# Kernel tuning notes

Hardware: AMD Instinct MI355X
Metric: run time of the kernel (lower is better)

The kernel has to match this reference:

```python
import math
import jax, jax.numpy as jnp
from jax import lax
import numpy as np

# ---- constants from init_kwargs / set_epoch(epoch=3) mid-warmstart-fade ----
B, T, K = 32, 262144, 64
BLEND = 0.5          # warmstart blend at epoch 3 (fade frac = 0.5)
LAM = 0.8            # current_lambda_* = lambda * (0.5 + 0.5*epoch/warmstart_epochs)
WINDOW = 20          # peakiness_window
SIGMA_BP = 50.0      # position_sigma_bp
TAG_WIDTH = 511.0    # tag_width_bp
S_MIN, S_MAX = 0.1, 1000.0
SCALE_PROBE = SCALE_BP = SCALE_VEL = SCALE_COUNT = 1.0
EPS = 1e-6


def setup_inputs() -> dict:
    key = jax.random.key(0)
    ks = jax.random.split(key, 8)
    pred_heatmap = jax.random.uniform(ks[0], (B, T), jnp.float32)
    # monotone cumulative bp positions per sample
    pred_cumulative_bp = jnp.cumsum(2.0 * jax.random.uniform(ks[1], (B, T), jnp.float32), axis=1)
    raw_velocity = jax.random.normal(ks[2], (B, T), jnp.float32)
    pred_heatmap_logits = jax.random.normal(ks[3], (B, T), jnp.float32)
    warmstart_heatmap = jax.random.uniform(ks[4], (B, T), jnp.float32)
    mask = jnp.ones((B, T), bool)
    # increasing reference bp positions, intervals in [500, 2500] bp
    ref_bp = jnp.cumsum(500.0 + 2000.0 * jax.random.uniform(ks[5], (B, K), jnp.float32), axis=1)
    gt_centers = jnp.sort(jax.random.randint(ks[6], (B, K), 0, T), axis=1).astype(jnp.int64)
    warmstart_valid = jnp.ones((B,), bool)
    n_ref_probes = jax.random.randint(ks[7], (B,), 2, K + 1).astype(jnp.int32)
    log_S = jnp.asarray(math.log(5.0), jnp.float32)  # learned scalar S_init=5.0
    return dict(pred_heatmap=pred_heatmap, pred_cumulative_bp=pred_cumulative_bp,
                raw_velocity=raw_velocity, pred_heatmap_logits=pred_heatmap_logits,
                warmstart_heatmap=warmstart_heatmap, ref_bp=ref_bp, log_S=log_S,
                mask=mask, gt_centers=gt_centers, warmstart_valid=warmstart_valid,
                n_ref_probes=n_ref_probes)


def _centernet_focal(logits, gt, maskf):
    # standard CenterNet focal loss, per sample  [B]
    p = jax.nn.sigmoid(logits)
    logp = jax.nn.log_sigmoid(logits)
    log1mp = jax.nn.log_sigmoid(-logits)
    pos = (gt >= 1.0).astype(logits.dtype)
    pos_term = ((1.0 - p) ** 2) * logp * pos
    neg_term = ((1.0 - gt) ** 4) * (p ** 2) * log1mp * (1.0 - pos)
    num_pos = jnp.maximum(jnp.sum(pos * maskf, axis=1), 1.0)
    return -jnp.sum((pos_term + neg_term) * maskf, axis=1) / num_pos


def _peakiness(mh):
    # fraction of heatmap mass NOT at local maxima within +/-WINDOW  [B]
    lmax = lax.reduce_window(mh, -jnp.inf, lax.max, (1, 2 * WINDOW + 1), (1, 1), 'SAME')
    ismax = (mh >= lmax).astype(mh.dtype)
    return 1.0 - jnp.sum(mh * ismax, axis=1) / (jnp.sum(mh, axis=1) + EPS)


def reference(pred_heatmap, pred_cumulative_bp, raw_velocity, pred_heatmap_logits,
              warmstart_heatmap, ref_bp, log_S, mask, gt_centers, warmstart_valid,
              n_ref_probes):
    f = pred_heatmap.dtype
    maskf = mask.astype(f)
    mh = pred_heatmap * maskf  # masked heatmap [B,T]

    # ---- probe component: blend*focal (if valid) + (1-blend)*peakiness ----
    focal = _centernet_focal(pred_heatmap_logits, warmstart_heatmap, maskf)
    peaky = _peakiness(mh)
    validf = warmstart_valid.astype(f)
    probe_loss = jnp.mean(BLEND * focal * validf + (1.0 - BLEND) * peaky)

    # ---- gather predicted cumulative bp at GT probe centers ----
    centers = jnp.clip(gt_centers, 0, T - 1)
    pred_at = jnp.take_along_axis(pred_cumulative_bp, centers, axis=1)  # [B,K]

    # ---- interval NLL with learned stretch noise scale S ----
    d_pred = jnp.diff(pred_at, axis=1)   # [B,K-1]
    d_ref = jnp.diff(ref_bp, axis=1)     # [B,K-1]
    S = jnp.clip(jnp.exp(log_S), S_MIN, S_MAX)
    v = jnp.sum(d_pred * d_ref, axis=1) / (jnp.sum(d_ref * d_ref, axis=1) + EPS)  # ML stretch [B]
    var = S * jnp.maximum(d_ref, 1.0)
    resid = d_pred - v[:, None] * d_ref
    bp_loss = jnp.mean(jnp.mean(0.5 * jnp.log(2.0 * math.pi * var) + resid ** 2 / (2.0 * var), axis=1))

    # ---- position (velocity) Gaussian NLL ----
    vel_nll = jnp.mean(0.5 * ((pred_at - ref_bp) / SIGMA_BP) ** 2, axis=1) \
        + math.log(SIGMA_BP * math.sqrt(2.0 * math.pi))
    vel_loss = jnp.mean(vel_nll)

    # ---- stretch prior: log-normal prior centered at v=1 ----
    stretch_prior_loss = jnp.mean(0.5 * jnp.log(jnp.clip(v, EPS)) ** 2)

    # ---- proximity-aware count loss ----
    ref_norm = jnp.abs(ref_bp - ref_bp[:, :1])
    ref_intervals = jnp.maximum(jnp.diff(ref_norm, axis=1), 1.0)
    resolvable = jnp.sum(jnp.minimum(lax.stop_gradient(ref_intervals) / TAG_WIDTH, 1.0), axis=1)
    n_ref_f = jnp.maximum(n_ref_probes, 2).astype(f)
    expected = jnp.minimum(n_ref_f, 1.0 + resolvable)
    pred_count = jnp.sum(mh, axis=1)
    count_loss = jnp.mean((pred_count - expected) ** 2 / (expected + 1.0))

    total = (probe_loss / SCALE_PROBE
             + LAM * bp_loss / SCALE_BP
             + LAM * vel_loss / SCALE_VEL
             + LAM * count_loss / SCALE_COUNT
             + LAM * stretch_prior_loss)
    return total
```

## Files before the change

kernel.cpp:

```cpp
#include <hip/hip_runtime.h>
#include <math.h>

#define B_  32
#define T_  262144
#define K_  64
#define NT  128


__device__ __forceinline__ float wred_sum(float v) {
#pragma unroll
    for (int m = 32; m > 0; m >>= 1) v += __shfl_xor(v, m);
    return v;
}

__device__ __forceinline__ float4 ld4g(const float* __restrict__ row, int off) {
    float4 v = make_float4(-INFINITY, -INFINITY, -INFINITY, -INFINITY);
    if ((unsigned)off < (unsigned)T_) v = *(const float4*)(row + off);
    return v;
}

__device__ __forceinline__ float max4(float4 u) {
    return fmaxf(fmaxf(u.x, u.y), fmaxf(u.z, u.w));
}

__global__ __launch_bounds__(256) void k_heatmap(
    const float* __restrict__ ph, const float* __restrict__ logits,
    const float* __restrict__ gt, float* __restrict__ ws)
{
    __shared__ float red[4][4];
    const int b    = blockIdx.y;
    const int t    = blockIdx.x;
    const int tid  = threadIdx.x;
    const int lane = tid & 63, wave = tid >> 6;
    const long rowoff = (long)b * T_;
    const float* row  = ph + rowoff;
    const int g = (t * 256 + tid) * 8;

    float4 x0 = *(const float4*)(row + g);
    float4 x1 = *(const float4*)(row + g + 4);
    float4 lv = ld4g(row, g - 20);
    float4 a0 = ld4g(row, g - 16);
    float4 a1 = ld4g(row, g - 12);
    float4 b0 = ld4g(row, g + 16);
    float4 b1 = ld4g(row, g + 20);
    float4 rv = ld4g(row, g + 24);
    const float4* lg4 = (const float4*)(logits + rowoff + g);
    const float4* gt4 = (const float4*)(gt     + rowoff + g);
    float4 f0 = lg4[0], f1 = lg4[1];
    float4 h0 = gt4[0], h1 = gt4[1];

    float m_edge = -INFINITY;
    if (lane == 0)  m_edge = fmaxf(max4(ld4g(row, g - 8)), max4(ld4g(row, g - 4)));
    if (lane == 63) m_edge = fmaxf(max4(ld4g(row, g + 8)), max4(ld4g(row, g + 12)));

    float x[8] = {x0.x, x0.y, x0.z, x0.w, x1.x, x1.y, x1.z, x1.w};
    float a[8] = {a0.x, a0.y, a0.z, a0.w, a1.x, a1.y, a1.z, a1.w};
    float bb[8] = {b0.x, b0.y, b0.z, b0.w, b1.x, b1.y, b1.z, b1.w};

    float M = fmaxf(max4(x0), max4(x1));

    float shm = __shfl(M, lane - 1);
    float Mm1 = (lane == 0)  ? m_edge : shm;
    float shp = __shfl(M, lane + 1);
    float Mp1 = (lane == 63) ? m_edge : shp;

    float s2[4];
    {
        float t7 = a[7];
        float t6 = fmaxf(a[6], t7), t5 = fmaxf(a[5], t6), t4 = fmaxf(a[4], t5);
        s2[3] = fmaxf(a[3], t4);
        s2[2] = fmaxf(a[2], s2[3]);
        s2[1] = fmaxf(a[1], s2[2]);
        s2[0] = fmaxf(a[0], s2[1]);
    }
    float p2[8];
    p2[0] = bb[0];
#pragma unroll
    for (int k = 1; k < 8; ++k) p2[k] = fmaxf(p2[k-1], bb[k]);
    float ls[4];
    ls[3] = lv.w; ls[2] = fmaxf(lv.z, ls[3]); ls[1] = fmaxf(lv.y, ls[2]); ls[0] = fmaxf(lv.x, ls[1]);
    float p3[4];
    p3[0] = rv.x; p3[1] = fmaxf(p3[0], rv.y); p3[2] = fmaxf(p3[1], rv.z); p3[3] = fmaxf(p3[2], rv.w);

    float mid3   = fmaxf(fmaxf(Mm1, M), Mp1);
    float mid_lo = fmaxf(mid3, s2[0]);
    float mid_hi = fmaxf(mid3, p2[7]);

    float sum_mh = 0.f, sum_peak = 0.f;
#pragma unroll
    for (int e = 0; e < 4; ++e) {
        float lmax = fmaxf(fmaxf(ls[e], mid_lo), p2[e + 4]);
        sum_mh += x[e];
        sum_peak += (x[e] >= lmax) ? x[e] : 0.f;
    }
#pragma unroll
    for (int e = 4; e < 8; ++e) {
        float lmax = fmaxf(fmaxf(s2[e - 4], mid_hi), p3[e - 4]);
        sum_mh += x[e];
        sum_peak += (x[e] >= lmax) ? x[e] : 0.f;
    }

    float fsum = 0.f, pcnt = 0.f;
    {
        float xs[8] = {f0.x, f0.y, f0.z, f0.w, f1.x, f1.y, f1.z, f1.w};
        float gs[8] = {h0.x, h0.y, h0.z, h0.w, h1.x, h1.y, h1.z, h1.w};
#pragma unroll
        for (int u = 0; u < 8; ++u) {
            float xv = xs[u], gv = gs[u];
            float q     = __expf(-fabsf(xv));
            float denom = 1.f + q;
            float rde   = __builtin_amdgcn_rcpf(denom);
            float L     = __logf(denom);
            float logp   = fminf(xv, 0.f) - L;
            float log1mp = logp - xv;
            float p      = ((xv >= 0.f) ? 1.f : q) * rde;
            float pos  = (gv >= 1.f) ? 1.f : 0.f;
            float omg  = 1.f - gv;
            float omg2 = omg * omg;
            float neg_term = omg2 * omg2 * p * p * log1mp;
            float omp  = 1.f - p;
            float pos_term = omp * omp * logp;
            fsum += pos * pos_term + (1.f - pos) * neg_term;
            pcnt += pos;
        }
    }

    sum_mh   = wred_sum(sum_mh);
    sum_peak = wred_sum(sum_peak);
    fsum     = wred_sum(fsum);
    pcnt     = wred_sum(pcnt);
    if (lane == 0) { red[wave][0] = sum_mh; red[wave][1] = sum_peak; red[wave][2] = fsum; red[wave][3] = pcnt; }
    __syncthreads();
    if (tid == 0) {
        float a0s = 0.f, a1s = 0.f, a2s = 0.f, a3s = 0.f;
        for (int w = 0; w < 4; ++w) { a0s += red[w][0]; a1s += red[w][1]; a2s += red[w][2]; a3s += red[w][3]; }
        ws[(0*B_ + b)*NT + t] = a0s;
        ws[(1*B_ + b)*NT + t] = a1s;
        ws[(2*B_ + b)*NT + t] = a2s;
        ws[(3*B_ + b)*NT + t] = a3s;
    }
}

__global__ __launch_bounds__(1024) void k_final(
    const float* __restrict__ pred_cum, const float* __restrict__ ref_bp,
    const float* __restrict__ log_S, const int* __restrict__ centers,
    const int* __restrict__ n_ref, const float* __restrict__ ws,
    float* __restrict__ out)
{
    __shared__ float acc_s[16];
    const int tid  = threadIdx.x;
    const int wave = tid >> 6, lane = tid & 63;

    float S = expf(log_S[0]);
    S = fminf(fmaxf(S, 0.1f), 1000.f);
    const float LOG_2PI = 1.8378770664093455f;
    const float VEL_C   = 4.8309615386328187f;

    float acc = 0.f;
    for (int b = wave; b < B_; b += 16) {
        float s_mh = wred_sum(ws[(0*B_+b)*NT + lane] + ws[(0*B_+b)*NT + lane + 64]);
        float s_pk = wred_sum(ws[(1*B_+b)*NT + lane] + ws[(1*B_+b)*NT + lane + 64]);
        float s_f  = wred_sum(ws[(2*B_+b)*NT + lane] + ws[(2*B_+b)*NT + lane + 64]);
        float s_pc = wred_sum(ws[(3*B_+b)*NT + lane] + ws[(3*B_+b)*NT + lane + 64]);

        int c = centers[b*K_ + lane];
        c = min(max(c, 0), T_ - 1);
        float pa = pred_cum[(long)b * T_ + c];
        float rb = ref_bp[b*K_ + lane];

        float pa1 = __shfl_down(pa, 1);
        float rb1 = __shfl_down(rb, 1);
        const bool v63 = (lane < 63);
        float dp = v63 ? (pa1 - pa) : 0.f;
        float dr = v63 ? (rb1 - rb) : 0.f;

        float num = wred_sum(dp * dr);
        float den = wred_sum(dr * dr);
        float v = num / (den + 1e-6f);

        float var   = S * fmaxf(dr, 1.f);
        float resid = dp - v * dr;
        float bp_t  = v63 ? (0.5f*(LOG_2PI + logf(var)) + resid*resid/(2.f*var)) : 0.f;
        float bp_b  = wred_sum(bp_t) * (1.f/63.f);

        float dv    = (pa - rb) * (1.f/50.f);
        float vel_b = wred_sum(0.5f*dv*dv) * (1.f/64.f) + VEL_C;

        float lv = logf(fmaxf(v, 1e-6f));
        float stretch_b = 0.5f * lv * lv;

        float rb0 = __shfl(rb, 0);
        float rn  = fabsf(rb - rb0);
        float rn1 = __shfl_down(rn, 1);
        float iv  = fmaxf(rn1 - rn, 1.f);
        float resolv = wred_sum(v63 ? fminf(iv * (1.f/511.f), 1.f) : 0.f);
        float nf   = fmaxf((float)n_ref[b], 2.f);
        float expd = fminf(nf, 1.f + resolv);
        float cdiff = s_mh - expd;
        float count_b = cdiff*cdiff / (expd + 1.f);

        float focal_b = -s_f / fmaxf(s_pc, 1.f);
        float peaky_b = 1.f - s_pk / (s_mh + 1e-6f);
        float probe_b = 0.5f * focal_b + 0.5f * peaky_b;

        acc += probe_b + 0.8f * (bp_b + vel_b + count_b + stretch_b);
    }

    if (lane == 0) acc_s[wave] = acc;
    __syncthreads();
    if (tid == 0) {
        float s = 0.f;
        for (int w = 0; w < 16; ++w) s += acc_s[w];
        out[0] = s * (1.f / (float)B_);
    }
}

extern "C" void kernel_launch(void* const* d_in, const int* in_sizes, int n_in,
                              void* d_out, int out_size, void* d_ws, size_t ws_size,
                              hipStream_t stream) {
    const float* ph = (const float*)d_in[0];
    const float* pc = (const float*)d_in[1];
    const float* lg = (const float*)d_in[3];
    const float* wh = (const float*)d_in[4];
    const float* rb = (const float*)d_in[5];
    const float* lS = (const float*)d_in[6];
    const int*   gc = (const int*)d_in[8];
    const int*   nr = (const int*)d_in[10];
    float* ws  = (float*)d_ws;
    float* out = (float*)d_out;

    hipLaunchKernelGGL(k_heatmap, dim3(NT, B_), dim3(256), 0, stream, ph, lg, wh, ws);
    hipLaunchKernelGGL(k_final,   dim3(1),      dim3(1024), 0, stream, pc, rb, lS, gc, nr, ws, out);
}
```

Baseline: 34.28 us.

## Fuse final reduction via last-block atomic counter and share window maxima through LDS

Merges the finalize kernel into the heatmap kernel: each block bumps a global atomic counter, and the last block to finish computes the scalar loss. This removes the second launch and its dependency gap. The sliding-window peak detection now builds per-thread prefix and suffix maxima in shared memory (XOR-swizzled addresses) and reads neighbours from there, instead of issuing six overlapping global float4 loads per thread. The counter is never reset; it relies on a modulo check of a counter that keeps growing across calls in the workspace. The finalize step now runs on only four waves, and the shared-memory staging adds a block barrier.

Measured after the change: 111.9 us. +226.5%, slower.

```diff
diff --git a/kernel.cpp b/kernel.cpp
--- a/kernel.cpp
+++ b/kernel.cpp
@@ -1,11 +1,12 @@
 #include <hip/hip_runtime.h>
 #include <math.h>
 
-#define B_  32
-#define T_  262144
-#define K_  64
-#define NT  128
-
+#define B_   32
+#define T_   262144
+#define K_   64
+#define NT   128
+#define NBLK (NT*B_)
+#define PART_FLOATS (4*B_*NT)
 
 __device__ __forceinline__ float wred_sum(float v) {
 #pragma unroll
@@ -18,16 +19,24 @@
     if ((unsigned)off < (unsigned)T_) v = *(const float4*)(row + off);
     return v;
 }
-
-__device__ __forceinline__ float max4(float4 u) {
-    return fmaxf(fmaxf(u.x, u.y), fmaxf(u.z, u.w));
-}
-
-__global__ __launch_bounds__(256) void k_heatmap(
+__device__ __forceinline__ float max4(float4 u) { return fmaxf(fmaxf(u.x, u.y), fmaxf(u.z, u.w)); }
+
+__device__ __forceinline__ int gaddr(int t, int q) {
+    return t * 16 + 4 * (q ^ ((t >> 1) & 3));
+}
+
+__global__ __launch_bounds__(256) void k_fused(
     const float* __restrict__ ph, const float* __restrict__ logits,
-    const float* __restrict__ gt, float* __restrict__ ws)
+    const float* __restrict__ gt, const float* __restrict__ pred_cum,
+    const float* __restrict__ ref_bp, const float* __restrict__ log_S,
+    const int* __restrict__ centers, const int* __restrict__ n_ref,
+    float* __restrict__ ws, unsigned int* __restrict__ counter,
+    float* __restrict__ out)
 {
+    __shared__ float sh[256 * 16];
     __shared__ float red[4][4];
+    __shared__ int   lastflag;
+
     const int b    = blockIdx.y;
     const int t    = blockIdx.x;
     const int tid  = threadIdx.x;
@@ -38,64 +47,72 @@
 
     float4 x0 = *(const float4*)(row + g);
     float4 x1 = *(const float4*)(row + g + 4);
-    float4 lv = ld4g(row, g - 20);
-    float4 a0 = ld4g(row, g - 16);
-    float4 a1 = ld4g(row, g - 12);
-    float4 b0 = ld4g(row, g + 16);
-    float4 b1 = ld4g(row, g + 20);
-    float4 rv = ld4g(row, g + 24);
     const float4* lg4 = (const float4*)(logits + rowoff + g);
     const float4* gt4 = (const float4*)(gt     + rowoff + g);
     float4 f0 = lg4[0], f1 = lg4[1];
     float4 h0 = gt4[0], h1 = gt4[1];
 
-    float m_edge = -INFINITY;
-    if (lane == 0)  m_edge = fmaxf(max4(ld4g(row, g - 8)), max4(ld4g(row, g - 4)));
-    if (lane == 63) m_edge = fmaxf(max4(ld4g(row, g + 8)), max4(ld4g(row, g + 12)));
-
     float x[8] = {x0.x, x0.y, x0.z, x0.w, x1.x, x1.y, x1.z, x1.w};
-    float a[8] = {a0.x, a0.y, a0.z, a0.w, a1.x, a1.y, a1.z, a1.w};
-    float bb[8] = {b0.x, b0.y, b0.z, b0.w, b1.x, b1.y, b1.z, b1.w};
-
-    float M = fmaxf(max4(x0), max4(x1));
-
-    float shm = __shfl(M, lane - 1);
-    float Mm1 = (lane == 0)  ? m_edge : shm;
-    float shp = __shfl(M, lane + 1);
-    float Mp1 = (lane == 63) ? m_edge : shp;
-
-    float s2[4];
-    {
-        float t7 = a[7];
-        float t6 = fmaxf(a[6], t7), t5 = fmaxf(a[5], t6), t4 = fmaxf(a[4], t5);
-        s2[3] = fmaxf(a[3], t4);
-        s2[2] = fmaxf(a[2], s2[3]);
-        s2[1] = fmaxf(a[1], s2[2]);
-        s2[0] = fmaxf(a[0], s2[1]);
-    }
-    float p2[8];
-    p2[0] = bb[0];
-#pragma unroll
-    for (int k = 1; k < 8; ++k) p2[k] = fmaxf(p2[k-1], bb[k]);
-    float ls[4];
-    ls[3] = lv.w; ls[2] = fmaxf(lv.z, ls[3]); ls[1] = fmaxf(lv.y, ls[2]); ls[0] = fmaxf(lv.x, ls[1]);
-    float p3[4];
-    p3[0] = rv.x; p3[1] = fmaxf(p3[0], rv.y); p3[2] = fmaxf(p3[1], rv.z); p3[3] = fmaxf(p3[2], rv.w);
-
-    float mid3   = fmaxf(fmaxf(Mm1, M), Mp1);
-    float mid_lo = fmaxf(mid3, s2[0]);
-    float mid_hi = fmaxf(mid3, p2[7]);
+
+    float P[8], Sx[8];
+    P[0] = x[0];
+#pragma unroll
+    for (int k = 1; k < 8; ++k) P[k] = fmaxf(P[k-1], x[k]);
+    Sx[7] = x[7];
+#pragma unroll
+    for (int k = 6; k >= 0; --k) Sx[k] = fmaxf(Sx[k+1], x[k]);
+
+    *(float4*)&sh[gaddr(tid, 0)] = make_float4(Sx[0], Sx[1], Sx[2], Sx[3]);
+    *(float4*)&sh[gaddr(tid, 1)] = make_float4(Sx[4], Sx[5], Sx[6], Sx[7]);
+    *(float4*)&sh[gaddr(tid, 2)] = make_float4(P[0],  P[1],  P[2],  P[3]);
+    *(float4*)&sh[gaddr(tid, 3)] = make_float4(P[4],  P[5],  P[6],  P[7]);
+    __syncthreads();
+
+    const int tm3 = max(tid-3, 0), tm2 = max(tid-2, 0), tm1 = max(tid-1, 0);
+    const int tp1 = min(tid+1, 255), tp2 = min(tid+2, 255), tp3 = min(tid+3, 255);
+    float4 lsv = *(const float4*)&sh[gaddr(tm3, 1)];
+    float4 s2v = *(const float4*)&sh[gaddr(tm2, 0)];
+    float4 p2v = *(const float4*)&sh[gaddr(tp2, 3)];
+    float4 p3v = *(const float4*)&sh[gaddr(tp3, 2)];
+    float  Mm1 = sh[gaddr(tm1, 3) + 3];
+    float  Mp1 = sh[gaddr(tp1, 3) + 3];
+
+    if (tid < 3) {
+        float4 lv = ld4g(row, g - 20);
+        float4 a0 = ld4g(row, g - 16), a1 = ld4g(row, g - 12);
+        lsv.w = lv.w; lsv.z = fmaxf(lv.z, lsv.w); lsv.y = fmaxf(lv.y, lsv.z); lsv.x = fmaxf(lv.x, lsv.y);
+        float t7 = a1.w, t6 = fmaxf(a1.z, t7), t5 = fmaxf(a1.y, t6), t4 = fmaxf(a1.x, t5);
+        s2v.w = fmaxf(a0.w, t4); s2v.z = fmaxf(a0.z, s2v.w); s2v.y = fmaxf(a0.y, s2v.z); s2v.x = fmaxf(a0.x, s2v.y);
+        Mm1 = fmaxf(max4(ld4g(row, g - 8)), max4(ld4g(row, g - 4)));
+    }
+    if (tid > 252) {
+        float4 b0 = ld4g(row, g + 16), b1 = ld4g(row, g + 20);
+        float4 rv = ld4g(row, g + 24);
+        float q0 = max4(b0);
+        p2v.x = fmaxf(q0, b1.x); p2v.y = fmaxf(p2v.x, b1.y); p2v.z = fmaxf(p2v.y, b1.z); p2v.w = fmaxf(p2v.z, b1.w);
+        p3v.x = rv.x; p3v.y = fmaxf(p3v.x, rv.y); p3v.z = fmaxf(p3v.y, rv.z); p3v.w = fmaxf(p3v.z, rv.w);
+        Mp1 = fmaxf(max4(ld4g(row, g + 8)), max4(ld4g(row, g + 12)));
+    }
+
+    const float M    = P[7];
+    const float mid3 = fmaxf(fmaxf(Mm1, M), Mp1);
+    const float mid_lo = fmaxf(mid3, s2v.x);
+    const float mid_hi = fmaxf(mid3, p2v.w);
+    float lsA[4] = {lsv.x, lsv.y, lsv.z, lsv.w};
+    float s2A[4] = {s2v.x, s2v.y, s2v.z, s2v.w};
+    float p2A[4] = {p2v.x, p2v.y, p2v.z, p2v.w};
+    float p3A[4] = {p3v.x, p3v.y, p3v.z, p3v.w};
 
     float sum_mh = 0.f, sum_peak = 0.f;
 #pragma unroll
     for (int e = 0; e < 4; ++e) {
-        float lmax = fmaxf(fmaxf(ls[e], mid_lo), p2[e + 4]);
+        float lmax = fmaxf(fmaxf(lsA[e], mid_lo), p2A[e]);
         sum_mh += x[e];
         sum_peak += (x[e] >= lmax) ? x[e] : 0.f;
     }
 #pragma unroll
     for (int e = 4; e < 8; ++e) {
-        float lmax = fmaxf(fmaxf(s2[e - 4], mid_hi), p3[e - 4]);
+        float lmax = fmaxf(fmaxf(s2A[e-4], mid_hi), p3A[e-4]);
         sum_mh += x[e];
         sum_peak += (x[e] >= lmax) ? x[e] : 0.f;
     }
@@ -138,80 +155,74 @@
         ws[(1*B_ + b)*NT + t] = a1s;
         ws[(2*B_ + b)*NT + t] = a2s;
         ws[(3*B_ + b)*NT + t] = a3s;
-    }
-}
-
-__global__ __launch_bounds__(1024) void k_final(
-    const float* __restrict__ pred_cum, const float* __restrict__ ref_bp,
-    const float* __restrict__ log_S, const int* __restrict__ centers,
-    const int* __restrict__ n_ref, const float* __restrict__ ws,
-    float* __restrict__ out)
-{
-    __shared__ float acc_s[16];
-    const int tid  = threadIdx.x;
-    const int wave = tid >> 6, lane = tid & 63;
-
-    float S = expf(log_S[0]);
-    S = fminf(fmaxf(S, 0.1f), 1000.f);
-    const float LOG_2PI = 1.8378770664093455f;
-    const float VEL_C   = 4.8309615386328187f;
-
-    float acc = 0.f;
-    for (int b = wave; b < B_; b += 16) {
-        float s_mh = wred_sum(ws[(0*B_+b)*NT + lane] + ws[(0*B_+b)*NT + lane + 64]);
-        float s_pk = wred_sum(ws[(1*B_+b)*NT + lane] + ws[(1*B_+b)*NT + lane + 64]);
-        float s_f  = wred_sum(ws[(2*B_+b)*NT + lane] + ws[(2*B_+b)*NT + lane + 64]);
-        float s_pc = wred_sum(ws[(3*B_+b)*NT + lane] + ws[(3*B_+b)*NT + lane + 64]);
-
-        int c = centers[b*K_ + lane];
-        c = min(max(c, 0), T_ - 1);
-        float pa = pred_cum[(long)b * T_ + c];
-        float rb = ref_bp[b*K_ + lane];
-
-        float pa1 = __shfl_down(pa, 1);
-        float rb1 = __shfl_down(rb, 1);
-        const bool v63 = (lane < 63);
-        float dp = v63 ? (pa1 - pa) : 0.f;
-        float dr = v63 ? (rb1 - rb) : 0.f;
-
-        float num = wred_sum(dp * dr);
-        float den = wred_sum(dr * dr);
-        float v = num / (den + 1e-6f);
-
-        float var   = S * fmaxf(dr, 1.f);
-        float resid = dp - v * dr;
-        float bp_t  = v63 ? (0.5f*(LOG_2PI + logf(var)) + resid*resid/(2.f*var)) : 0.f;
-        float bp_b  = wred_sum(bp_t) * (1.f/63.f);
-
-        float dv    = (pa - rb) * (1.f/50.f);
-        float vel_b = wred_sum(0.5f*dv*dv) * (1.f/64.f) + VEL_C;
-
-        float lv = logf(fmaxf(v, 1e-6f));
-        float stretch_b = 0.5f * lv * lv;
-
-        float rb0 = __shfl(rb, 0);
-        float rn  = fabsf(rb - rb0);
-        float rn1 = __shfl_down(rn, 1);
-        float iv  = fmaxf(rn1 - rn, 1.f);
-        float resolv = wred_sum(v63 ? fminf(iv * (1.f/511.f), 1.f) : 0.f);
-        float nf   = fmaxf((float)n_ref[b], 2.f);
-        float expd = fminf(nf, 1.f + resolv);
-        float cdiff = s_mh - expd;
-        float count_b = cdiff*cdiff / (expd + 1.f);
-
-        float focal_b = -s_f / fmaxf(s_pc, 1.f);
-        float peaky_b = 1.f - s_pk / (s_mh + 1e-6f);
-        float probe_b = 0.5f * focal_b + 0.5f * peaky_b;
-
-        acc += probe_b + 0.8f * (bp_b + vel_b + count_b + stretch_b);
-    }
-
-    if (lane == 0) acc_s[wave] = acc;
+        __threadfence();
+        unsigned int old = atomicAdd(counter, 1u);
+        lastflag = ((old & (NBLK - 1)) == (NBLK - 1));
+    }
     __syncthreads();
-    if (tid == 0) {
-        float s = 0.f;
-        for (int w = 0; w < 16; ++w) s += acc_s[w];
-        out[0] = s * (1.f / (float)B_);
+
+    if (lastflag) {
+        __threadfence();
+
+        float S = expf(log_S[0]);
+        S = fminf(fmaxf(S, 0.1f), 1000.f);
+        const float LOG_2PI = 1.8378770664093455f;
+        const float VEL_C   = 4.8309615386328187f;
+
+        float acc = 0.f;
+        for (int bb = wave; bb < B_; bb += 4) {
+            float s_mh = wred_sum(ws[(0*B_+bb)*NT + lane] + ws[(0*B_+bb)*NT + lane + 64]);
+            float s_pk = wred_sum(ws[(1*B_+bb)*NT + lane] + ws[(1*B_+bb)*NT + lane + 64]);
+            float s_f  = wred_sum(ws[(2*B_+bb)*NT + lane] + ws[(2*B_+bb)*NT + lane + 64]);
+            float s_pc = wred_sum(ws[(3*B_+bb)*NT + lane] + ws[(3*B_+bb)*NT + lane + 64]);
+
+            int c = centers[bb*K_ + lane];
+            c = min(max(c, 0), T_ - 1);
+            float pa = pred_cum[(long)bb * T_ + c];
+            float rb = ref_bp[bb*K_ + lane];
+
+            float pa1 = __shfl_down(pa, 1);
+            float rb1 = __shfl_down(rb, 1);
+            const bool v63 = (lane < 63);
+            float dp = v63 ? (pa1 - pa) : 0.f;
+            float dr = v63 ? (rb1 - rb) : 0.f;
+
+            float num = wred_sum(dp * dr);
+            float den = wred_sum(dr * dr);
+            float v = num / (den + 1e-6f);
+
+            float var   = S * fmaxf(dr, 1.f);
+            float resid = dp - v * dr;
+            float bp_t  = v63 ? (0.5f*(LOG_2PI + logf(var)) + resid*resid/(2.f*var)) : 0.f;
+            float bp_b  = wred_sum(bp_t) * (1.f/63.f);
+
+            float dv    = (pa - rb) * (1.f/50.f);
+            float vel_b = wred_sum(0.5f*dv*dv) * (1.f/64.f) + VEL_C;
+
+            float lv2 = logf(fmaxf(v, 1e-6f));
+            float stretch_b = 0.5f * lv2 * lv2;
+
+            float rb0 = __shfl(rb, 0);
+            float rn  = fabsf(rb - rb0);
+            float rn1 = __shfl_down(rn, 1);
+            float iv  = fmaxf(rn1 - rn, 1.f);
+            float resolv = wred_sum(v63 ? fminf(iv * (1.f/511.f), 1.f) : 0.f);
+            float nf   = fmaxf((float)n_ref[bb], 2.f);
+            float expd = fminf(nf, 1.f + resolv);
+            float cdiff = s_mh - expd;
+            float count_b = cdiff*cdiff / (expd + 1.f);
+
+            float focal_b = -s_f / fmaxf(s_pc, 1.f);
+            float peaky_b = 1.f - s_pk / (s_mh + 1e-6f);
+            float probe_b = 0.5f * focal_b + 0.5f * peaky_b;
+
+            acc += probe_b + 0.8f * (bp_b + vel_b + count_b + stretch_b);
+        }
+
+        if (lane == 0) red[wave][0] = acc;
+        __syncthreads();
+        if (tid == 0)
+            out[0] = (red[0][0] + red[1][0] + red[2][0] + red[3][0]) * (1.f / (float)B_);
     }
 }
 
@@ -227,8 +238,9 @@
     const int*   gc = (const int*)d_in[8];
     const int*   nr = (const int*)d_in[10];
     float* ws  = (float*)d_ws;
+    unsigned int* counter = (unsigned int*)((char*)d_ws + PART_FLOATS * sizeof(float));
     float* out = (float*)d_out;
 
-    hipLaunchKernelGGL(k_heatmap, dim3(NT, B_), dim3(256), 0, stream, ph, lg, wh, ws);
-    hipLaunchKernelGGL(k_final,   dim3(1),      dim3(1024), 0, stream, pc, rb, lS, gc, nr, ws, out);
-}
+    hipLaunchKernelGGL(k_fused, dim3(NT, B_), dim3(256), 0, stream,
+                       ph, lg, wh, pc, rb, lS, gc, nr, ws, counter, out);
+}
```

## Double per-thread elements and share window prefix/suffix maxima through LDS

Applied to the files above, without the earlier changes.

Each thread now handles 16 elements instead of 8, halving the block count. The sliding-window max halo, previously fetched with redundant global loads, is now built from neighbouring threads' prefix and suffix maxima exchanged through swizzled shared memory, with only the block-edge threads loading halo data from global memory. This removes overlapping halo reads but adds an LDS round-trip and a barrier, lowers the number of waves in flight, and raises register pressure.

After: 33.54 us. 2.1% less time.

```diff
diff --git a/kernel.cpp b/kernel.cpp
--- a/kernel.cpp
+++ b/kernel.cpp
@@ -1,10 +1,13 @@
 #include <hip/hip_runtime.h>
 #include <math.h>
 
-#define B_  32
-#define T_  262144
-#define K_  64
-#define NT  128
+#define B_   32
+#define T_   262144
+#define K_   64
+#define TPB  256
+#define ELEM 16
+#define TILE_ (TPB*ELEM)
+#define NT   (T_/TILE_)
 
 
 __device__ __forceinline__ float wred_sum(float v) {
@@ -19,93 +22,129 @@
     return v;
 }
 
-__device__ __forceinline__ float max4(float4 u) {
-    return fmaxf(fmaxf(u.x, u.y), fmaxf(u.z, u.w));
+__device__ __forceinline__ int gaddr(int t, int q) {
+    return t * 32 + 4 * (q ^ (t & 7));
 }
 
 __global__ __launch_bounds__(256) void k_heatmap(
     const float* __restrict__ ph, const float* __restrict__ logits,
     const float* __restrict__ gt, float* __restrict__ ws)
 {
+    __shared__ float sh[TPB * 32];
     __shared__ float red[4][4];
+
     const int b    = blockIdx.y;
     const int t    = blockIdx.x;
     const int tid  = threadIdx.x;
     const int lane = tid & 63, wave = tid >> 6;
     const long rowoff = (long)b * T_;
     const float* row  = ph + rowoff;
-    const int g = (t * 256 + tid) * 8;
-
-    float4 x0 = *(const float4*)(row + g);
-    float4 x1 = *(const float4*)(row + g + 4);
-    float4 lv = ld4g(row, g - 20);
-    float4 a0 = ld4g(row, g - 16);
-    float4 a1 = ld4g(row, g - 12);
-    float4 b0 = ld4g(row, g + 16);
-    float4 b1 = ld4g(row, g + 20);
-    float4 rv = ld4g(row, g + 24);
+    const int g = (t * TPB + tid) * ELEM;
+
+    float4 v0 = *(const float4*)(row + g);
+    float4 v1 = *(const float4*)(row + g + 4);
+    float4 v2 = *(const float4*)(row + g + 8);
+    float4 v3 = *(const float4*)(row + g + 12);
+    float x[16] = {v0.x,v0.y,v0.z,v0.w, v1.x,v1.y,v1.z,v1.w,
+                   v2.x,v2.y,v2.z,v2.w, v3.x,v3.y,v3.z,v3.w};
+
+    float P[16], Sx[16];
+    P[0] = x[0];
+#pragma unroll
+    for (int k = 1; k < 16; ++k) P[k] = fmaxf(P[k-1], x[k]);
+    Sx[15] = x[15];
+#pragma unroll
+    for (int k = 14; k >= 0; --k) Sx[k] = fmaxf(Sx[k+1], x[k]);
+
+#pragma unroll
+    for (int q = 0; q < 4; ++q)
+        *(float4*)&sh[gaddr(tid, q)] = make_float4(Sx[4*q], Sx[4*q+1], Sx[4*q+2], Sx[4*q+3]);
+#pragma unroll
+    for (int q = 0; q < 4; ++q)
+        *(float4*)&sh[gaddr(tid, 4+q)] = make_float4(P[4*q], P[4*q+1], P[4*q+2], P[4*q+3]);
+    __syncthreads();
+
     const float4* lg4 = (const float4*)(logits + rowoff + g);
     const float4* gt4 = (const float4*)(gt     + rowoff + g);
-    float4 f0 = lg4[0], f1 = lg4[1];
-    float4 h0 = gt4[0], h1 = gt4[1];
-
-    float m_edge = -INFINITY;
-    if (lane == 0)  m_edge = fmaxf(max4(ld4g(row, g - 8)), max4(ld4g(row, g - 4)));
-    if (lane == 63) m_edge = fmaxf(max4(ld4g(row, g + 8)), max4(ld4g(row, g + 12)));
-
-    float x[8] = {x0.x, x0.y, x0.z, x0.w, x1.x, x1.y, x1.z, x1.w};
-    float a[8] = {a0.x, a0.y, a0.z, a0.w, a1.x, a1.y, a1.z, a1.w};
-    float bb[8] = {b0.x, b0.y, b0.z, b0.w, b1.x, b1.y, b1.z, b1.w};
-
-    float M = fmaxf(max4(x0), max4(x1));
-
-    float shm = __shfl(M, lane - 1);
-    float Mm1 = (lane == 0)  ? m_edge : shm;
-    float shp = __shfl(M, lane + 1);
-    float Mp1 = (lane == 63) ? m_edge : shp;
-
-    float s2[4];
-    {
-        float t7 = a[7];
-        float t6 = fmaxf(a[6], t7), t5 = fmaxf(a[5], t6), t4 = fmaxf(a[4], t5);
-        s2[3] = fmaxf(a[3], t4);
-        s2[2] = fmaxf(a[2], s2[3]);
-        s2[1] = fmaxf(a[1], s2[2]);
-        s2[0] = fmaxf(a[0], s2[1]);
-    }
-    float p2[8];
-    p2[0] = bb[0];
-#pragma unroll
-    for (int k = 1; k < 8; ++k) p2[k] = fmaxf(p2[k-1], bb[k]);
-    float ls[4];
-    ls[3] = lv.w; ls[2] = fmaxf(lv.z, ls[3]); ls[1] = fmaxf(lv.y, ls[2]); ls[0] = fmaxf(lv.x, ls[1]);
-    float p3[4];
-    p3[0] = rv.x; p3[1] = fmaxf(p3[0], rv.y); p3[2] = fmaxf(p3[1], rv.z); p3[3] = fmaxf(p3[2], rv.w);
-
-    float mid3   = fmaxf(fmaxf(Mm1, M), Mp1);
-    float mid_lo = fmaxf(mid3, s2[0]);
-    float mid_hi = fmaxf(mid3, p2[7]);
+    float4 f0 = lg4[0], f1 = lg4[1], f2 = lg4[2], f3 = lg4[3];
+    float4 h0 = gt4[0], h1 = gt4[1], h2 = gt4[2], h3 = gt4[3];
+
+    const int tm1 = max(tid-1, 0), tm2 = max(tid-2, 0);
+    const int tp1 = min(tid+1, TPB-1), tp2 = min(tid+2, TPB-1);
+    float4 sxA = *(const float4*)&sh[gaddr(tm1, 0)];
+    float4 sxB = *(const float4*)&sh[gaddr(tm1, 1)];
+    float4 sxC = *(const float4*)&sh[gaddr(tm1, 2)];
+    float4 sx2 = *(const float4*)&sh[gaddr(tm2, 3)];
+    float4 pB  = *(const float4*)&sh[gaddr(tp1, 5)];
+    float4 pC  = *(const float4*)&sh[gaddr(tp1, 6)];
+    float4 pD  = *(const float4*)&sh[gaddr(tp1, 7)];
+    float4 p2  = *(const float4*)&sh[gaddr(tp2, 4)];
+
+    if (tid == 0) {
+        float u[20];
+        float4 a = ld4g(row, g-20), bq = ld4g(row, g-16), c = ld4g(row, g-12),
+               d = ld4g(row, g-8),  e = ld4g(row, g-4);
+        u[0]=a.x;u[1]=a.y;u[2]=a.z;u[3]=a.w; u[4]=bq.x;u[5]=bq.y;u[6]=bq.z;u[7]=bq.w;
+        u[8]=c.x;u[9]=c.y;u[10]=c.z;u[11]=c.w; u[12]=d.x;u[13]=d.y;u[14]=d.z;u[15]=d.w;
+        u[16]=e.x;u[17]=e.y;u[18]=e.z;u[19]=e.w;
+        float ss[20];
+        ss[19] = u[19];
+#pragma unroll
+        for (int k = 18; k >= 0; --k) ss[k] = fmaxf(u[k], ss[k+1]);
+        sx2 = make_float4(ss[0], ss[1], ss[2], ss[3]);
+        sxA = make_float4(ss[4], ss[5], ss[6], ss[7]);
+        sxB = make_float4(ss[8], ss[9], ss[10], ss[11]);
+        sxC = make_float4(ss[12], ss[13], ss[14], ss[15]);
+    } else if (tid == 1) {
+        float4 lv = ld4g(row, g - 20);
+        float s3 = lv.w, s2s = fmaxf(lv.z, s3), s1s = fmaxf(lv.y, s2s), s0s = fmaxf(lv.x, s1s);
+        sx2 = make_float4(s0s, s1s, s2s, s3);
+    }
+    if (tid == TPB-1) {
+        float u[20];
+        float4 a = ld4g(row, g+16), bq = ld4g(row, g+20), c = ld4g(row, g+24),
+               d = ld4g(row, g+28), e = ld4g(row, g+32);
+        u[0]=a.x;u[1]=a.y;u[2]=a.z;u[3]=a.w; u[4]=bq.x;u[5]=bq.y;u[6]=bq.z;u[7]=bq.w;
+        u[8]=c.x;u[9]=c.y;u[10]=c.z;u[11]=c.w; u[12]=d.x;u[13]=d.y;u[14]=d.z;u[15]=d.w;
+        u[16]=e.x;u[17]=e.y;u[18]=e.z;u[19]=e.w;
+        float pp[20];
+        pp[0] = u[0];
+#pragma unroll
+        for (int k = 1; k < 20; ++k) pp[k] = fmaxf(pp[k-1], u[k]);
+        pB = make_float4(pp[4], pp[5], pp[6], pp[7]);
+        pC = make_float4(pp[8], pp[9], pp[10], pp[11]);
+        pD = make_float4(pp[12], pp[13], pp[14], pp[15]);
+        p2 = make_float4(pp[16], pp[17], pp[18], pp[19]);
+    } else if (tid == TPB-2) {
+        float4 rv = ld4g(row, g + 32);
+        float q0 = rv.x, q1 = fmaxf(q0, rv.y), q2 = fmaxf(q1, rv.z), q3 = fmaxf(q2, rv.w);
+        p2 = make_float4(q0, q1, q2, q3);
+    }
+
+    float S1a[12] = {sxA.x,sxA.y,sxA.z,sxA.w, sxB.x,sxB.y,sxB.z,sxB.w, sxC.x,sxC.y,sxC.z,sxC.w};
+    float PPa[12] = {pB.x,pB.y,pB.z,pB.w, pC.x,pC.y,pC.z,pC.w, pD.x,pD.y,pD.z,pD.w};
+    float sx2a[4] = {sx2.x, sx2.y, sx2.z, sx2.w};
+    float p2a[4]  = {p2.x,  p2.y,  p2.z,  p2.w};
+    const float M = P[15];
 
     float sum_mh = 0.f, sum_peak = 0.f;
 #pragma unroll
-    for (int e = 0; e < 4; ++e) {
-        float lmax = fmaxf(fmaxf(ls[e], mid_lo), p2[e + 4]);
+    for (int e = 0; e < 16; ++e) {
+        float left  = (e < 4)  ? fmaxf(sx2a[e], S1a[0]) : S1a[e-4];
+        float right = (e < 12) ? PPa[e] : fmaxf(PPa[11], p2a[e-12]);
+        float lmax  = fmaxf(fmaxf(left, M), right);
         sum_mh += x[e];
         sum_peak += (x[e] >= lmax) ? x[e] : 0.f;
     }
-#pragma unroll
-    for (int e = 4; e < 8; ++e) {
-        float lmax = fmaxf(fmaxf(s2[e - 4], mid_hi), p3[e - 4]);
-        sum_mh += x[e];
-        sum_peak += (x[e] >= lmax) ? x[e] : 0.f;
-    }
 
     float fsum = 0.f, pcnt = 0.f;
     {
-        float xs[8] = {f0.x, f0.y, f0.z, f0.w, f1.x, f1.y, f1.z, f1.w};
-        float gs[8] = {h0.x, h0.y, h0.z, h0.w, h1.x, h1.y, h1.z, h1.w};
-#pragma unroll
-        for (int u = 0; u < 8; ++u) {
+        float xs[16] = {f0.x,f0.y,f0.z,f0.w, f1.x,f1.y,f1.z,f1.w,
+                        f2.x,f2.y,f2.z,f2.w, f3.x,f3.y,f3.z,f3.w};
+        float gs[16] = {h0.x,h0.y,h0.z,h0.w, h1.x,h1.y,h1.z,h1.w,
+                        h2.x,h2.y,h2.z,h2.w, h3.x,h3.y,h3.z,h3.w};
+#pragma unroll
+        for (int u = 0; u < 16; ++u) {
             float xv = xs[u], gv = gs[u];
             float q     = __expf(-fabsf(xv));
             float denom = 1.f + q;
@@ -132,8 +171,8 @@
     if (lane == 0) { red[wave][0] = sum_mh; red[wave][1] = sum_peak; red[wave][2] = fsum; red[wave][3] = pcnt; }
     __syncthreads();
     if (tid == 0) {
-        float a0s = 0.f, a1s = 0.f, a2s = 0.f, a3s = 0.f;
-        for (int w = 0; w < 4; ++w) { a0s += red[w][0]; a1s += red[w][1]; a2s += red[w][2]; a3s += red[w][3]; }
+        float a0s=0.f, a1s=0.f, a2s=0.f, a3s=0.f;
+        for (int w = 0; w < 4; ++w) { a0s+=red[w][0]; a1s+=red[w][1]; a2s+=red[w][2]; a3s+=red[w][3]; }
         ws[(0*B_ + b)*NT + t] = a0s;
         ws[(1*B_ + b)*NT + t] = a1s;
         ws[(2*B_ + b)*NT + t] = a2s;
@@ -158,10 +197,10 @@
 
     float acc = 0.f;
     for (int b = wave; b < B_; b += 16) {
-        float s_mh = wred_sum(ws[(0*B_+b)*NT + lane] + ws[(0*B_+b)*NT + lane + 64]);
-        float s_pk = wred_sum(ws[(1*B_+b)*NT + lane] + ws[(1*B_+b)*NT + lane + 64]);
-        float s_f  = wred_sum(ws[(2*B_+b)*NT + lane] + ws[(2*B_+b)*NT + lane + 64]);
-        float s_pc = wred_sum(ws[(3*B_+b)*NT + lane] + ws[(3*B_+b)*NT + lane + 64]);
+        float s_mh = wred_sum(lane < NT ? ws[(0*B_+b)*NT + lane] : 0.f);
+        float s_pk = wred_sum(lane < NT ? ws[(1*B_+b)*NT + lane] : 0.f);
+        float s_f  = wred_sum(lane < NT ? ws[(2*B_+b)*NT + lane] : 0.f);
+        float s_pc = wred_sum(lane < NT ? ws[(3*B_+b)*NT + lane] : 0.f);
 
         int c = centers[b*K_ + lane];
         c = min(max(c, 0), T_ - 1);
@@ -229,6 +268,6 @@
     float* ws  = (float*)d_ws;
     float* out = (float*)d_out;
 
-    hipLaunchKernelGGL(k_heatmap, dim3(NT, B_), dim3(256), 0, stream, ph, lg, wh, ws);
+    hipLaunchKernelGGL(k_heatmap, dim3(NT, B_), dim3(TPB), 0, stream, ph, lg, wh, ws);
     hipLaunchKernelGGL(k_final,   dim3(1),      dim3(1024), 0, stream, pc, rb, lS, gc, nr, ws, out);
 }
```
